# Kernel optimization log

Measured on AMD Instinct MI355X. Metric: run time of the kernel, lower is better.

The kernel has to match this reference:

```python
import jax, jax.numpy as jnp
import numpy as np

B, N, C, H = 2, 2048, 1024, 16
D = C // H
EPS = 1e-6
SCALE = D ** -0.5


def _ln(x, w, b):
    m = jnp.mean(x, axis=-1, keepdims=True)
    v = jnp.var(x, axis=-1, keepdims=True)
    return (x - m) * jax.lax.rsqrt(v + EPS) * w + b


def setup_inputs() -> dict:
    key = jax.random.key(0)
    ks = jax.random.split(key, 10)
    s = 0.02
    return {
        "hidden_states": jax.random.normal(ks[0], (B, N, C), jnp.float32),
        "attention_mask": jnp.ones((B, N), dtype=bool),
        "pos_embeds": jax.random.normal(ks[1], (B, N, C), jnp.float32),
        "Wq": jax.random.normal(ks[2], (C, C), jnp.float32) * s,
        "bq": jnp.zeros((C,), jnp.float32),
        "Wk": jax.random.normal(ks[3], (C, C), jnp.float32) * s,
        "bk": jnp.zeros((C,), jnp.float32),
        "Wv": jax.random.normal(ks[4], (C, C), jnp.float32) * s,
        "bv": jnp.zeros((C,), jnp.float32),
        "Wo": jax.random.normal(ks[5], (C, C), jnp.float32) * s,
        "bo": jnp.zeros((C,), jnp.float32),
        "q_ln_w": jnp.ones((C,), jnp.float32),
        "q_ln_b": jnp.zeros((C,), jnp.float32),
        "k_ln_w": jnp.ones((C,), jnp.float32),
        "k_ln_b": jnp.zeros((C,), jnp.float32),
        "Wp": jax.random.normal(ks[6], (C, C), jnp.float32) * s,  # linear_pos, no bias
        "pos_bias_u": jax.random.normal(ks[7], (H, D), jnp.float32) * s,
        "pos_bias_v": jax.random.normal(ks[8], (H, D), jnp.float32) * s,
    }


def reference(hidden_states, attention_mask, pos_embeds, Wq, bq, Wk, bk, Wv, bv,
              Wo, bo, q_ln_w, q_ln_b, k_ln_w, k_ln_b, Wp, pos_bias_u, pos_bias_v):
    x = hidden_states  # (B,N,C)
    # projections; QK-LayerNorm is applied over the flattened (H*D)=C dim,
    # which equals LN on the projected (B,N,C) tensors before the head split.
    q = _ln(x @ Wq.T + bq, q_ln_w, q_ln_b).reshape(B, N, H, D)
    k = _ln(x @ Wk.T + bk, k_ln_w, k_ln_b).reshape(B, N, H, D)
    v = (x @ Wv.T + bv).reshape(B, N, H, D)
    p = (pos_embeds @ Wp.T).reshape(B, N, H, D)
    # Transformer-XL ac + bd terms
    matrix_ac = jnp.einsum('bnhd,bmhd->bhnm', q + pos_bias_u, k)
    matrix_bd = jnp.einsum('bnhd,bmhd->bhnm', q + pos_bias_v, p)
    attn = (matrix_ac + matrix_bd) * SCALE
    mask = attention_mask[:, None, None, :]  # (B,1,1,N) over key dim
    attn = jnp.where(mask, attn, -jnp.inf)
    attn = jax.nn.softmax(attn, axis=-1)
    out = jnp.einsum('bhnm,bmhd->bnhd', attn, v).reshape(B, N, C)
    return out @ Wo.T + bo
```

## Files before the change

### kernel.cpp

```cpp
#include <hip/hip_runtime.h>
#include <stdint.h>


typedef short short8 __attribute__((ext_vector_type(8)));
typedef float f32x4 __attribute__((ext_vector_type(4)));
typedef unsigned short us4 __attribute__((ext_vector_type(4)));
typedef unsigned short u16;

#define NB 2
#define NN 2048
#define NC 1024
#define NH 16
#define ND 64

__device__ __forceinline__ u16 f2bf(float f) {
    unsigned int u = __float_as_uint(f);
    u += 0x7fffu + ((u >> 16) & 1u);
    return (u16)(u >> 16);
}

__device__ __forceinline__ int swzc(int row, int c) {
    return (((c >> 3) ^ (row & 7)) << 3) | (c & 7);
}

__device__ __forceinline__ void gload16(const void* g, void* l) {
    __builtin_amdgcn_global_load_lds(
        (const __attribute__((address_space(1))) unsigned int*)g,
        (__attribute__((address_space(3))) unsigned int*)l, 16, 0, 0);
}

__global__ __launch_bounds__(256) void cast_kernel(const float* __restrict__ src,
                                                   u16* __restrict__ dst, int n4) {
    int i = blockIdx.x * 256 + threadIdx.x;
    if (i < n4) {
        float4 f = reinterpret_cast<const float4*>(src)[i];
        us4 o;
        o[0] = f2bf(f.x); o[1] = f2bf(f.y); o[2] = f2bf(f.z); o[3] = f2bf(f.w);
        reinterpret_cast<us4*>(dst)[i] = o;
    }
}

__device__ __forceinline__ void gemm_stage(const u16* __restrict__ A,
                                           const u16* __restrict__ W,
                                           u16* As, u16* Bs,
                                           int m0, int n0, int kk, int w, int lane) {
    int lr4 = lane >> 2, lc8 = (lane & 3) * 8;
#pragma unroll
    for (int i = 0; i < 2; i++) {
        int rbase = w * 32 + i * 16;
        gload16(A + (size_t)(m0 + rbase + lr4) * 1024 + kk + lc8, As + rbase * 32);
        gload16(W + (size_t)(n0 + rbase + lr4) * 1024 + kk + lc8, Bs + rbase * 32);
    }
}

__device__ __forceinline__ void gemm_bt_body(const u16* __restrict__ A,
                                             const u16* __restrict__ W,
                                             float* __restrict__ out,
                                             const float* __restrict__ bias,
                                             int m0, int n0) {
    __shared__ u16 As[2][128 * 32];
    __shared__ u16 Bs[2][128 * 32];
    int t = threadIdx.x, lane = t & 63, w = t >> 6;
    int wm = (w >> 1) * 64, wn = (w & 1) * 64;
    int lr = lane & 15, lg = lane >> 4;
    f32x4 acc[4][4] = {};

    gemm_stage(A, W, As[0], Bs[0], m0, n0, 0, w, lane);
    __syncthreads();
    int cur = 0;
    for (int kt = 0; kt < 32; kt++) {
        if (kt < 31)
            gemm_stage(A, W, As[cur ^ 1], Bs[cur ^ 1], m0, n0, (kt + 1) * 32, w, lane);
        const u16* Ac = As[cur];
        const u16* Bc = Bs[cur];
        short8 af[4], bw[4];
#pragma unroll
        for (int mt = 0; mt < 4; mt++)
            af[mt] = *reinterpret_cast<const short8*>(Ac + (wm + mt * 16 + lr) * 32 + lg * 8);
#pragma unroll
        for (int nt = 0; nt < 4; nt++)
            bw[nt] = *reinterpret_cast<const short8*>(Bs[cur] + (wn + nt * 16 + lr) * 32 + lg * 8);
#pragma unroll
        for (int mt = 0; mt < 4; mt++)
#pragma unroll
            for (int nt = 0; nt < 4; nt++)
                acc[mt][nt] = __builtin_amdgcn_mfma_f32_16x16x32_bf16(af[mt], bw[nt], acc[mt][nt], 0, 0, 0);
        __syncthreads();
        cur ^= 1;
    }
#pragma unroll
    for (int mt = 0; mt < 4; mt++) {
#pragma unroll
        for (int nt = 0; nt < 4; nt++) {
            int c = n0 + wn + nt * 16 + lr;
            float badd = bias ? bias[c] : 0.0f;
            int r = m0 + wm + mt * 16 + lg * 4;
#pragma unroll
            for (int rg = 0; rg < 4; rg++)
                out[(size_t)(r + rg) * 1024 + c] = acc[mt][nt][rg] + badd;
        }
    }
}

__global__ __launch_bounds__(256) void proj_gemm(const u16* __restrict__ xbf,
                                                 const u16* __restrict__ posbf,
                                                 const u16* __restrict__ Wbase,
                                                 float* __restrict__ prebase,
                                                 const float* __restrict__ bq,
                                                 const float* __restrict__ bk,
                                                 const float* __restrict__ bv) {
    int z = blockIdx.z;
    const u16* A = (z == 3) ? posbf : xbf;
    const u16* W = Wbase + (size_t)z * 1048576;
    float* out = prebase + (size_t)z * 4194304;
    const float* bias = (z == 0) ? bq : ((z == 1) ? bk : ((z == 2) ? bv : (const float*)nullptr));
    gemm_bt_body(A, W, out, bias, blockIdx.y * 128, blockIdx.x * 128);
}

__global__ __launch_bounds__(256) void out_gemm(const u16* __restrict__ ctx,
                                                const u16* __restrict__ Wo,
                                                float* __restrict__ out,
                                                const float* __restrict__ bo) {
    gemm_bt_body(ctx, Wo, out, bo, blockIdx.y * 128, blockIdx.x * 128);
}

__global__ __launch_bounds__(256) void post_qk(const float* __restrict__ prebase,
                                               const float* __restrict__ qw, const float* __restrict__ qb,
                                               const float* __restrict__ kw, const float* __restrict__ kb,
                                               const float* __restrict__ pbu, const float* __restrict__ pbv,
                                               u16* __restrict__ QQ, u16* __restrict__ KK) {
    const float QSC = 0.125f * 1.44269504089f;
    int isq = (blockIdx.y == 0);
    const float* pre = prebase + (isq ? 0 : (size_t)4194304);
    const float* lw = isq ? qw : kw;
    const float* lb = isq ? qb : kb;
    int wv = threadIdx.x >> 6, lane = threadIdx.x & 63;
    int row = blockIdx.x * 4 + wv;
    int b = row >> 11, n = row & 2047;
    const float* pr = pre + (size_t)row * 1024;
    float vals[16];
    float s = 0.f, s2 = 0.f;
#pragma unroll
    for (int i = 0; i < 4; i++) {
        float4 f = *reinterpret_cast<const float4*>(pr + i * 256 + lane * 4);
        vals[i * 4 + 0] = f.x; vals[i * 4 + 1] = f.y; vals[i * 4 + 2] = f.z; vals[i * 4 + 3] = f.w;
        s += f.x + f.y + f.z + f.w;
        s2 += f.x * f.x + f.y * f.y + f.z * f.z + f.w * f.w;
    }
#pragma unroll
    for (int m = 1; m < 64; m <<= 1) { s += __shfl_xor(s, m); s2 += __shfl_xor(s2, m); }
    float mean = s * (1.f / 1024.f);
    float var = s2 * (1.f / 1024.f) - mean * mean;
    float inv = rsqrtf(var + 1e-6f);
#pragma unroll
    for (int i = 0; i < 4; i++) {
        int c0 = i * 256 + lane * 4;
        int h = c0 >> 6, d0 = c0 & 63;
        size_t base = ((size_t)(b * NH + h) * NN + n) * 128;
        if (isq) {
            us4 u0, u1;
#pragma unroll
            for (int j = 0; j < 4; j++) {
                float xn = (vals[i * 4 + j] - mean) * inv * lw[c0 + j] + lb[c0 + j];
                u0[j] = f2bf((xn + pbu[h * 64 + d0 + j]) * QSC);
                u1[j] = f2bf((xn + pbv[h * 64 + d0 + j]) * QSC);
            }
            *reinterpret_cast<us4*>(QQ + base + swzc(n, d0)) = u0;
            *reinterpret_cast<us4*>(QQ + base + swzc(n, d0 + 64)) = u1;
        } else {
            us4 u0;
#pragma unroll
            for (int j = 0; j < 4; j++) {
                float xn = (vals[i * 4 + j] - mean) * inv * lw[c0 + j] + lb[c0 + j];
                u0[j] = f2bf(xn);
            }
            *reinterpret_cast<us4*>(KK + base + swzc(n, d0)) = u0;
        }
    }
}

__global__ __launch_bounds__(256) void post_vp(const float* __restrict__ vpre,
                                               const float* __restrict__ ppre,
                                               u16* __restrict__ Vt, u16* __restrict__ KK) {
    __shared__ u16 tile[64][66];
    int bh = blockIdx.x;
    int b = bh >> 4, h = bh & 15;
    int n0 = blockIdx.y * 64;
    int t = threadIdx.x, lane = t & 63, w = t >> 6;
#pragma unroll
    for (int j = 0; j < 4; j++) {
        int nr = t >> 2;
        int d = (t & 3) * 16 + j * 4;
        int n = n0 + nr;
        size_t goff = ((size_t)(b * NN + n)) * 1024 + h * 64 + d;
        float4 fv = *reinterpret_cast<const float4*>(vpre + goff);
        tile[nr][d + 0] = f2bf(fv.x);
        tile[nr][d + 1] = f2bf(fv.y);
        tile[nr][d + 2] = f2bf(fv.z);
        tile[nr][d + 3] = f2bf(fv.w);
        float4 fp = *reinterpret_cast<const float4*>(ppre + goff);
        us4 up; up[0] = f2bf(fp.x); up[1] = f2bf(fp.y); up[2] = f2bf(fp.z); up[3] = f2bf(fp.w);
        *reinterpret_cast<us4*>(KK + ((size_t)(b * NH + h) * NN + n) * 128 + swzc(n, 64 + d)) = up;
    }
    __syncthreads();
    size_t vbase = (size_t)(b * NH + h) * 64 * NN;
    int n = n0 + lane;
#pragma unroll
    for (int j = 0; j < 16; j++) {
        int d = w + j * 4;
        int nsw = (n & ~63) | ((((n >> 3) & 7) ^ (d & 7)) << 3) | (n & 7);
        Vt[vbase + (size_t)d * NN + nsw] = tile[lane][d];
    }
}

__global__ __launch_bounds__(512, 4) void flash_attn(const u16* __restrict__ QQ,
                                                     const u16* __restrict__ KK,
                                                     const u16* __restrict__ Vt,
                                                     u16* __restrict__ ctx) {
    __shared__ u16 KQs[2 * 64 * 128];
    __shared__ u16 Vts[2 * 64 * 64];
    __shared__ u16 Ps[8 * 16 * 64];
    int qt = blockIdx.x, h = blockIdx.y, b = blockIdx.z;
    int n0 = qt * 128;
    int t = threadIdx.x, lane = t & 63, w = t >> 6;
    int lr = lane & 15, lg = lane >> 4;
    const char* QQg = (const char*)(QQ + ((size_t)(b * NH + h) * NN) * 128);
    const char* KKg = (const char*)(KK + ((size_t)(b * NH + h) * NN) * 128);
    const char* Vtg = (const char*)(Vt + ((size_t)(b * NH + h) * 64) * NN);

#pragma unroll
    for (int i = 0; i < 4; i++)
        gload16(QQg + (size_t)n0 * 256 + i * 8192 + w * 1024 + lane * 16,
                (char*)KQs + i * 8192 + w * 1024);
    __syncthreads();
    short8 aq[4];
    {
        int row = w * 16 + lr;
#pragma unroll
        for (int ks = 0; ks < 4; ks++)
            aq[ks] = *reinterpret_cast<const short8*>(
                KQs + row * 128 + (((ks * 4 + lg) ^ (row & 7)) << 3));
    }
    __syncthreads();

#pragma unroll
    for (int i = 0; i < 2; i++)
        gload16(KKg + i * 8192 + w * 1024 + lane * 16, (char*)KQs + i * 8192 + w * 1024);
    gload16(Vtg + (size_t)(w * 8 + (lane >> 3)) * (NN * 2) + (lane & 7) * 16,
            (char*)Vts + w * 1024);
    __syncthreads();

    f32x4 O[4] = {};
    float mrun[4], lrun[4];
#pragma unroll
    for (int rg = 0; rg < 4; rg++) { mrun[rg] = -1e30f; lrun[rg] = 0.f; }

    int cur = 0;
    for (int tt = 0; tt < 32; tt++) {
        if (tt < 31) {
            int m1 = (tt + 1) * 64;
            int nb = cur ^ 1;
#pragma unroll
            for (int i = 0; i < 2; i++)
                gload16(KKg + (size_t)m1 * 256 + i * 8192 + w * 1024 + lane * 16,
                        (char*)KQs + nb * 16384 + i * 8192 + w * 1024);
            gload16(Vtg + (size_t)(w * 8 + (lane >> 3)) * (NN * 2) + (size_t)m1 * 2 + (lane & 7) * 16,
                    (char*)Vts + nb * 8192 + w * 1024);
        }
        const u16* Kc = KQs + cur * 8192;
        const u16* Vc = Vts + cur * 4096;
        f32x4 S[4];
        __builtin_amdgcn_s_setprio(1);
#pragma unroll
        for (int ct = 0; ct < 4; ct++) {
            f32x4 s = {};
#pragma unroll
            for (int ks = 0; ks < 4; ks++) {
                int row = ct * 16 + lr;
                short8 bk = *reinterpret_cast<const short8*>(
                    Kc + row * 128 + (((ks * 4 + lg) ^ (row & 7)) << 3));
                s = __builtin_amdgcn_mfma_f32_16x16x32_bf16(aq[ks], bk, s, 0, 0, 0);
            }
            S[ct] = s;
        }
        __builtin_amdgcn_s_setprio(0);
#pragma unroll
        for (int rg = 0; rg < 4; rg++) {
            float mx = fmaxf(fmaxf(S[0][rg], S[1][rg]), fmaxf(S[2][rg], S[3][rg]));
#pragma unroll
            for (int mk = 1; mk < 16; mk <<= 1) mx = fmaxf(mx, __shfl_xor(mx, mk));
            float newm = fmaxf(mrun[rg], mx);
            float sf = exp2f(mrun[rg] - newm);
            float ls = 0.f;
#pragma unroll
            for (int ct = 0; ct < 4; ct++) {
                float p = exp2f(S[ct][rg] - newm);
                S[ct][rg] = p;
                ls += p;
            }
#pragma unroll
            for (int mk = 1; mk < 16; mk <<= 1) ls += __shfl_xor(ls, mk);
            lrun[rg] = lrun[rg] * sf + ls;
            mrun[rg] = newm;
#pragma unroll
            for (int dt = 0; dt < 4; dt++) O[dt][rg] *= sf;
        }
        u16* Pw = Ps + w * 1024;
#pragma unroll
        for (int ct = 0; ct < 4; ct++) {
            int c = ct * 16 + lr;
#pragma unroll
            for (int rg = 0; rg < 4; rg++) {
                int row = lg * 4 + rg;
                Pw[row * 64 + ((((c >> 3) ^ (row & 7)) << 3) | (c & 7))] = f2bf(S[ct][rg]);
            }
        }
        short8 pa[2];
#pragma unroll
        for (int ks = 0; ks < 2; ks++)
            pa[ks] = *reinterpret_cast<const short8*>(
                Pw + lr * 64 + (((ks * 4 + lg) ^ (lr & 7)) << 3));
        __builtin_amdgcn_s_setprio(1);
#pragma unroll
        for (int dt = 0; dt < 4; dt++) {
#pragma unroll
            for (int ks = 0; ks < 2; ks++) {
                int vrow = dt * 16 + lr;
                short8 vf = *reinterpret_cast<const short8*>(
                    Vc + vrow * 64 + (((ks * 4 + lg) ^ (vrow & 7)) << 3));
                O[dt] = __builtin_amdgcn_mfma_f32_16x16x32_bf16(pa[ks], vf, O[dt], 0, 0, 0);
            }
        }
        __builtin_amdgcn_s_setprio(0);
        __syncthreads();
        cur ^= 1;
    }
#pragma unroll
    for (int dt = 0; dt < 4; dt++) {
#pragma unroll
        for (int rg = 0; rg < 4; rg++) {
            int n = n0 + w * 16 + lg * 4 + rg;
            float oo = O[dt][rg] / lrun[rg];
            ctx[((size_t)(b * NN) + n) * 1024 + h * 64 + dt * 16 + lr] = f2bf(oo);
        }
    }
}

extern "C" void kernel_launch(void* const* d_in, const int* in_sizes, int n_in,
                              void* d_out, int out_size, void* d_ws, size_t ws_size,
                              hipStream_t stream) {
    const float* x   = (const float*)d_in[0];
    const float* pos = (const float*)d_in[2];
    const float* Wq  = (const float*)d_in[3];
    const float* bq  = (const float*)d_in[4];
    const float* Wk  = (const float*)d_in[5];
    const float* bk  = (const float*)d_in[6];
    const float* Wv  = (const float*)d_in[7];
    const float* bv  = (const float*)d_in[8];
    const float* Wo  = (const float*)d_in[9];
    const float* bo  = (const float*)d_in[10];
    const float* qlw = (const float*)d_in[11];
    const float* qlb = (const float*)d_in[12];
    const float* klw = (const float*)d_in[13];
    const float* klb = (const float*)d_in[14];
    const float* Wp  = (const float*)d_in[15];
    const float* pbu = (const float*)d_in[16];
    const float* pbv = (const float*)d_in[17];
    float* out = (float*)d_out;

    char* ws = (char*)d_ws;
    u16*   xbf   = (u16*)(ws);
    u16*   posbf = (u16*)(ws + 8388608);
    u16*   Wbf   = (u16*)(ws + 16777216);
    float* pre   = (float*)(ws + 27262976);
    u16*   QQ    = (u16*)(ws + 94371840);
    u16*   KK    = (u16*)(ws + 111149056);
    u16*   Vt    = (u16*)(ws + 127926272);
    u16*   ctx   = (u16*)(ws + 136314880);

    cast_kernel<<<4096, 256, 0, stream>>>(x, xbf, 1048576);
    cast_kernel<<<4096, 256, 0, stream>>>(pos, posbf, 1048576);
    cast_kernel<<<1024, 256, 0, stream>>>(Wq, Wbf + 0 * 1048576, 262144);
    cast_kernel<<<1024, 256, 0, stream>>>(Wk, Wbf + 1 * 1048576, 262144);
    cast_kernel<<<1024, 256, 0, stream>>>(Wv, Wbf + 2 * 1048576, 262144);
    cast_kernel<<<1024, 256, 0, stream>>>(Wp, Wbf + 3 * 1048576, 262144);
    cast_kernel<<<1024, 256, 0, stream>>>(Wo, Wbf + 4 * 1048576, 262144);

    proj_gemm<<<dim3(8, 32, 4), 256, 0, stream>>>(xbf, posbf, Wbf, pre, bq, bk, bv);
    post_qk<<<dim3(1024, 2), 256, 0, stream>>>(pre, qlw, qlb, klw, klb, pbu, pbv, QQ, KK);
    post_vp<<<dim3(32, 32), 256, 0, stream>>>(pre + (size_t)2 * 4194304, pre + (size_t)3 * 4194304, Vt, KK);
    flash_attn<<<dim3(16, 16, 2), 512, 0, stream>>>(QQ, KK, Vt, ctx);
    out_gemm<<<dim3(8, 32), 256, 0, stream>>>(ctx, Wbf + 4 * 1048576, out, bo);
}
```

Measured before the change: 261.2 us.

## Use lazy softmax rescaling and compute row sums via MFMA with ones vector

The online softmax now rescales the output accumulator only when some row's new max exceeds the running max by more than a threshold (wave-uniform branch), skipping the exp and multiply work in most iterations. The per-row sum of probabilities is computed by an extra MFMA against a vector of bf16 ones instead of a shuffle-reduction, which also makes the denominator consistent with the bf16-rounded P. This trades two extra MFMAs per tile for removing the sum shuffles and most rescale work, and lets unnormalized exponentials grow up to 2^8, which is safe in fp32.

```diff
diff --git a/kernel.cpp b/kernel.cpp
--- a/kernel.cpp
+++ b/kernel.cpp
@@ -79,7 +79,7 @@
             af[mt] = *reinterpret_cast<const short8*>(Ac + (wm + mt * 16 + lr) * 32 + lg * 8);
 #pragma unroll
         for (int nt = 0; nt < 4; nt++)
-            bw[nt] = *reinterpret_cast<const short8*>(Bs[cur] + (wn + nt * 16 + lr) * 32 + lg * 8);
+            bw[nt] = *reinterpret_cast<const short8*>(Bc + (wn + nt * 16 + lr) * 32 + lg * 8);
 #pragma unroll
         for (int mt = 0; mt < 4; mt++)
 #pragma unroll
@@ -228,6 +228,10 @@
     const char* KKg = (const char*)(KK + ((size_t)(b * NH + h) * NN) * 128);
     const char* Vtg = (const char*)(Vt + ((size_t)(b * NH + h) * 64) * NN);
 
+    short8 vones;
+#pragma unroll
+    for (int i = 0; i < 8; i++) vones[i] = (short)0x3F80;
+
 #pragma unroll
     for (int i = 0; i < 4; i++)
         gload16(QQg + (size_t)n0 * 256 + i * 8192 + w * 1024 + lane * 16,
@@ -251,9 +255,10 @@
     __syncthreads();
 
     f32x4 O[4] = {};
-    float mrun[4], lrun[4];
-#pragma unroll
-    for (int rg = 0; rg < 4; rg++) { mrun[rg] = -1e30f; lrun[rg] = 0.f; }
+    f32x4 O5 = {};
+    float mrun[4];
+#pragma unroll
+    for (int rg = 0; rg < 4; rg++) mrun[rg] = -1e30f;
 
     int cur = 0;
     for (int tt = 0; tt < 32; tt++) {
@@ -284,26 +289,26 @@
             S[ct] = s;
         }
         __builtin_amdgcn_s_setprio(0);
+        float mx[4];
 #pragma unroll
         for (int rg = 0; rg < 4; rg++) {
-            float mx = fmaxf(fmaxf(S[0][rg], S[1][rg]), fmaxf(S[2][rg], S[3][rg]));
-#pragma unroll
-            for (int mk = 1; mk < 16; mk <<= 1) mx = fmaxf(mx, __shfl_xor(mx, mk));
-            float newm = fmaxf(mrun[rg], mx);
-            float sf = exp2f(mrun[rg] - newm);
-            float ls = 0.f;
-#pragma unroll
-            for (int ct = 0; ct < 4; ct++) {
-                float p = exp2f(S[ct][rg] - newm);
-                S[ct][rg] = p;
-                ls += p;
-            }
-#pragma unroll
-            for (int mk = 1; mk < 16; mk <<= 1) ls += __shfl_xor(ls, mk);
-            lrun[rg] = lrun[rg] * sf + ls;
-            mrun[rg] = newm;
-#pragma unroll
-            for (int dt = 0; dt < 4; dt++) O[dt][rg] *= sf;
+            float m0 = fmaxf(fmaxf(S[0][rg], S[1][rg]), fmaxf(S[2][rg], S[3][rg]));
+#pragma unroll
+            for (int mk = 1; mk < 16; mk <<= 1) m0 = fmaxf(m0, __shfl_xor(m0, mk));
+            mx[rg] = m0;
+        }
+        bool need = (mx[0] > mrun[0] + 8.f) || (mx[1] > mrun[1] + 8.f) ||
+                    (mx[2] > mrun[2] + 8.f) || (mx[3] > mrun[3] + 8.f);
+        if (__any(need)) {
+#pragma unroll
+            for (int rg = 0; rg < 4; rg++) {
+                float newm = fmaxf(mrun[rg], mx[rg]);
+                float sf = exp2f(mrun[rg] - newm);
+                mrun[rg] = newm;
+#pragma unroll
+                for (int dt = 0; dt < 4; dt++) O[dt][rg] *= sf;
+                O5[rg] *= sf;
+            }
         }
         u16* Pw = Ps + w * 1024;
 #pragma unroll
@@ -312,7 +317,8 @@
 #pragma unroll
             for (int rg = 0; rg < 4; rg++) {
                 int row = lg * 4 + rg;
-                Pw[row * 64 + ((((c >> 3) ^ (row & 7)) << 3) | (c & 7))] = f2bf(S[ct][rg]);
+                Pw[row * 64 + ((((c >> 3) ^ (row & 7)) << 3) | (c & 7))] =
+                    f2bf(exp2f(S[ct][rg] - mrun[rg]));
             }
         }
         short8 pa[2];
@@ -331,6 +337,9 @@
                 O[dt] = __builtin_amdgcn_mfma_f32_16x16x32_bf16(pa[ks], vf, O[dt], 0, 0, 0);
             }
         }
+#pragma unroll
+        for (int ks = 0; ks < 2; ks++)
+            O5 = __builtin_amdgcn_mfma_f32_16x16x32_bf16(pa[ks], vones, O5, 0, 0, 0);
         __builtin_amdgcn_s_setprio(0);
         __syncthreads();
         cur ^= 1;
@@ -340,7 +349,7 @@
 #pragma unroll
         for (int rg = 0; rg < 4; rg++) {
             int n = n0 + w * 16 + lg * 4 + rg;
-            float oo = O[dt][rg] / lrun[rg];
+            float oo = O[dt][rg] / O5[rg];
             ctx[((size_t)(b * NN) + n) * 1024 + h * 64 + dt * 16 + lr] = f2bf(oo);
         }
     }
```

Result: faster. 243.7 us (-6.7%).
